# Kernel optimization log

Hardware: AMD Instinct MI355X
Metric: run time of the kernel (lower is better)

Reference implementation:

```python
import jax, jax.numpy as jnp
import numpy as np
from jax import lax

B = 64


def _conv_bn_relu(x, w, cb, s, t):
    # 3x3 conv pad=1 (SAME), eval-mode BN folded to per-channel scale s / shift t, ReLU
    y = lax.conv_general_dilated(x, w, (1, 1), 'SAME',
                                 dimension_numbers=('NCHW', 'OIHW', 'NCHW'))
    y = y + cb[None, :, None, None]
    y = y * s[None, :, None, None] + t[None, :, None, None]
    return jax.nn.relu(y)


def _maxpool(x, k):
    return lax.reduce_window(x, -jnp.inf, lax.max, (1, 1, k, k), (1, 1, k, k), 'VALID')


def _tensor_dlt(H4PT, CornerA):
    # Batched version of the per-sample 8x8 DLT solve (faithful to the original row layout)
    U = CornerA[:, 0::2]            # [B,4]
    V = CornerA[:, 1::2]
    Ud = U + H4PT[:, 0::2]
    Vd = V + H4PT[:, 1::2]
    z = jnp.zeros_like(U)
    o = jnp.ones_like(U)
    r0 = jnp.stack([z, z, z, -U, V, -o, Vd * U, Vd * V], axis=-1)   # [B,4,8]
    r1 = jnp.stack([U, V, o, z, z, z, -Ud * U, -Ud * V], axis=-1)   # [B,4,8]
    A = jnp.stack([r0, r1], axis=2).reshape(U.shape[0], 8, 8)        # interleave rows per point
    bvec = jnp.stack([-Vd, Ud], axis=2).reshape(U.shape[0], 8)
    h = jnp.linalg.solve(A, bvec[..., None])[..., 0]                 # [B,8]
    H = jnp.concatenate([h, jnp.ones((U.shape[0], 1), h.dtype)], axis=1)
    return H.reshape(-1, 3, 3)


def _bilinear_sample(img, xs, ys):
    # img [Hs,Ws]; xs, ys [Ho,Wo]; zeros padding outside (grid_sample semantics)
    Hs, Ws = img.shape
    x0 = jnp.floor(xs)
    y0 = jnp.floor(ys)
    wx = xs - x0
    wy = ys - y0
    x0i = x0.astype(jnp.int32)
    y0i = y0.astype(jnp.int32)

    def gat(yi, xi):
        valid = (xi >= 0) & (xi < Ws) & (yi >= 0) & (yi < Hs)
        v = img[jnp.clip(yi, 0, Hs - 1), jnp.clip(xi, 0, Ws - 1)]
        return jnp.where(valid, v, jnp.zeros((), img.dtype))

    v00 = gat(y0i, x0i)
    v01 = gat(y0i, x0i + 1)
    v10 = gat(y0i + 1, x0i)
    v11 = gat(y0i + 1, x0i + 1)
    return (v00 * (1 - wx) * (1 - wy) + v01 * wx * (1 - wy)
            + v10 * (1 - wx) * wy + v11 * wx * wy)


def _warp_perspective(imgs, Hm, out_hw=(128, 128)):
    # dst(x,y) = src(H^{-1} [x,y,1]); align_corners=True pixel coordinates
    Ho, Wo = out_hw
    dt = imgs.dtype
    ys, xs = jnp.meshgrid(jnp.arange(Ho, dtype=dt), jnp.arange(Wo, dtype=dt), indexing='ij')
    grid = jnp.stack([xs, ys, jnp.ones_like(xs)], axis=-1)           # [Ho,Wo,3]
    Hinv = jnp.linalg.inv(Hm)                                        # [B,3,3]
    pts = jnp.einsum('bij,hwj->bhwi', Hinv, grid)                    # [B,Ho,Wo,3]
    xs_s = pts[..., 0] / pts[..., 2]
    ys_s = pts[..., 1] / pts[..., 2]
    out = jax.vmap(_bilinear_sample)(imgs, xs_s, ys_s)               # [B,Ho,Wo]
    return out[:, None]                                              # [B,1,Ho,Wo]


def setup_inputs() -> dict:
    key = jax.random.key(0)
    ks = jax.random.split(key, 64)
    d = {}
    d['TCropABatch'] = jax.random.uniform(ks[0], (B, 128, 128), jnp.float32)
    d['TI1Batch'] = jax.random.uniform(ks[1], (B, 2, 128, 128), jnp.float32)
    d['TImgABatch'] = jax.random.uniform(ks[2], (B, 240, 320), jnp.float32)
    # corners of a 128x128 quad inside the 240x320 image: (x,y) per corner, 8 values
    x0 = jax.random.uniform(ks[3], (B,), jnp.float32, 0.0, 192.0)
    y0 = jax.random.uniform(ks[4], (B,), jnp.float32, 0.0, 112.0)
    d['TCornerBatch'] = jnp.stack(
        [x0, y0, x0 + 127.0, y0, x0, y0 + 127.0, x0 + 127.0, y0 + 127.0], axis=1)
    chans = [(2, 64), (64, 64), (64, 64), (64, 64), (64, 128), (128, 128), (128, 128), (128, 128)]
    ki = 5
    for i, (ci, co) in enumerate(chans, start=1):
        fan = ci * 9
        d[f'w{i}'] = jax.random.normal(ks[ki], (co, ci, 3, 3), jnp.float32) * np.float32((2.0 / fan) ** 0.5)
        d[f'cb{i}'] = jnp.zeros((co,), jnp.float32)
        d[f's{i}'] = jnp.ones((co,), jnp.float32) + 0.01 * jax.random.normal(ks[ki + 1], (co,), jnp.float32)
        d[f't{i}'] = 0.01 * jax.random.normal(ks[ki + 2], (co,), jnp.float32)
        ki += 3
    d['fcw'] = jax.random.normal(ks[ki], (1024, 512), jnp.float32) * 0.02
    d['fcb'] = jnp.zeros((1024,), jnp.float32)
    d['f1w'] = jax.random.normal(ks[ki + 1], (8, 1024), jnp.float32) * 0.01
    d['f1b'] = jnp.zeros((8,), jnp.float32)
    return d


def reference(TCropABatch, TI1Batch, TImgABatch, TCornerBatch,
              w1, cb1, s1, t1, w2, cb2, s2, t2, w3, cb3, s3, t3, w4, cb4, s4, t4,
              w5, cb5, s5, t5, w6, cb6, s6, t6, w7, cb7, s7, t7, w8, cb8, s8, t8,
              fcw, fcb, f1w, f1b):
    ws = [w1, w2, w3, w4, w5, w6, w7, w8]
    cbs = [cb1, cb2, cb3, cb4, cb5, cb6, cb7, cb8]
    ss = [s1, s2, s3, s4, s5, s6, s7, s8]
    ts = [t1, t2, t3, t4, t5, t6, t7, t8]
    pools = [None, 2, None, 2, None, 2, None, 6]
    out = TI1Batch
    for i in range(8):
        out = _conv_bn_relu(out, ws[i], cbs[i], ss[i], ts[i])
        if pools[i] is not None:
            out = _maxpool(out, pools[i])
    out = out.reshape(out.shape[0], -1)                 # [B,512]
    out = jax.nn.relu(out @ fcw.T + fcb)                # dropout is eval-mode identity
    H4PT = out @ f1w.T + f1b                            # [B,8]
    Hm = _tensor_dlt(H4PT, TCornerBatch)                # [B,3,3]
    b_Pred = _warp_perspective(TImgABatch, Hm)          # [B,1,128,128]
    return b_Pred
```

## Files before the change

### kernel.cpp

```cpp
#include <hip/hip_runtime.h>
#include <math.h>

typedef __attribute__((ext_vector_type(4))) float f32x4;
typedef __attribute__((ext_vector_type(8))) short sh8;

__device__ __forceinline__ float bf2f(unsigned short u){
    union { unsigned int i; float f; } v; v.i = ((unsigned)u) << 16; return v.f;
}
__device__ __forceinline__ unsigned short f2bf(float f){
    union { float f; unsigned int i; } v; v.f = f;
    unsigned int x = v.i;
    x += 0x7fff + ((x >> 16) & 1);
    return (unsigned short)(x >> 16);
}

struct WTArgs {
    const float* src[7];
    unsigned short* hi[7];
    int cin[7];
    int start[8];
};

__global__ void wtrans_all(WTArgs a)
{
    int e = blockIdx.x * 256 + threadIdx.x;
    if (e >= a.start[7]) return;
    int l = 0;
    while (e >= a.start[l + 1]) l++;
    int eL = e - a.start[l];
    int CIN = a.cin[l];
    int tap = eL % 9, rest = eL / 9;
    int ci = rest % CIN, co = rest / CIN;
    int COUT = (a.start[l + 1] - a.start[l]) / (9 * CIN);
    a.hi[l][(tap * COUT + co) * CIN + ci] = f2bf(a.src[l][eL]);
}

__global__ __launch_bounds__(256) void conv1_kernel(
    const float* __restrict__ in, const float* __restrict__ w,
    const float* __restrict__ cb, const float* __restrict__ sc,
    const float* __restrict__ tb, unsigned short* __restrict__ out)
{
    __shared__ float s_w[18 * 64];
    __shared__ float s_in[2][18 * 20];

    const int tid = threadIdx.x;
    const int b = blockIdx.y;
    const int tile = blockIdx.x;
    const int ty = tile >> 3, tx = tile & 7;
    const int y0 = ty * 16, x0 = tx * 16;

    for (int idx = tid; idx < 1152; idx += 256) {
        int co = idx & 63, kk2 = idx >> 6;
        s_w[kk2 * 64 + co] = w[co * 18 + kk2];
    }
    for (int idx = tid; idx < 2 * 324; idx += 256) {
        int ci = idx / 324, rem = idx % 324;
        int r = rem / 18, c = rem % 18;
        int gy = y0 + r - 1, gx = x0 + c - 1;
        float v = 0.f;
        if (gy >= 0 && gy < 128 && gx >= 0 && gx < 128)
            v = in[((size_t)(b * 2 + ci) * 128 + gy) * 128 + gx];
        s_in[ci][r * 20 + c] = v;
    }
    __syncthreads();

    const int cog = tid >> 5;
    const int slot = tid & 31;
    const int sy = slot >> 2, sx = slot & 3;

    float p[2][4][6];
#pragma unroll
    for (int ci = 0; ci < 2; ci++)
#pragma unroll
        for (int r = 0; r < 4; r++)
#pragma unroll
            for (int c = 0; c < 6; c++)
                p[ci][r][c] = s_in[ci][(2 * sy + r) * 20 + 4 * sx + c];

    float acc[2][4][8];
#pragma unroll
    for (int r = 0; r < 2; r++)
#pragma unroll
        for (int c = 0; c < 4; c++)
#pragma unroll
            for (int o = 0; o < 8; o++) acc[r][c][o] = 0.f;

#pragma unroll
    for (int kk2 = 0; kk2 < 18; kk2++) {
        const int ci = kk2 / 9, k = kk2 % 9;
        const int ky = k / 3, kx = k % 3;
        float wv[8];
#pragma unroll
        for (int q = 0; q < 2; q++) {
            f32x4 w4 = *(const f32x4*)(&s_w[kk2 * 64 + cog * 8 + q * 4]);
#pragma unroll
            for (int z = 0; z < 4; z++) wv[q * 4 + z] = w4[z];
        }
#pragma unroll
        for (int r = 0; r < 2; r++)
#pragma unroll
            for (int c = 0; c < 4; c++) {
                float pv = p[ci][r + ky][c + kx];
#pragma unroll
                for (int o = 0; o < 8; o++) acc[r][c][o] += pv * wv[o];
            }
    }

    float bb[8], ss[8], tt[8];
#pragma unroll
    for (int o = 0; o < 8; o++) { bb[o] = cb[cog*8+o]; ss[o] = sc[cog*8+o]; tt[o] = tb[cog*8+o]; }
#pragma unroll
    for (int r = 0; r < 2; r++)
#pragma unroll
        for (int c = 0; c < 4; c++) {
            unsigned short ov[8];
#pragma unroll
            for (int o = 0; o < 8; o++)
                ov[o] = f2bf(fmaxf((acc[r][c][o] + bb[o]) * ss[o] + tt[o], 0.f));
            int py = y0 + 2 * sy + r, px = x0 + 4 * sx + c;
            *(sh8*)(out + ((size_t)(b * 128 + py) * 128 + px) * 64 + cog * 8) = *(sh8*)ov;
        }
}

template<int CIN, int COUT, int HI, int WI, int POOL, int TW, int NPG, int KSPLIT>
__global__ __launch_bounds__(NPG * 128, 4) void conv_mfma(
    const unsigned short* __restrict__ in,
    const unsigned short* __restrict__ wgt,
    const float* __restrict__ cb, const float* __restrict__ sc,
    const float* __restrict__ tb, void* __restrict__ outv)
{
    constexpr int THREADS = NPG * 128;
    constexpr int TH = (TW == 32) ? 2 * NPG : 4 * NPG;
    constexpr int HALW = TW + 2, HALH = TH + 2;
    constexpr int NPIX = HALW * HALH;
    constexpr int CHUNKS = CIN / 64;
    constexpr int TILESX = WI / TW;
    constexpr int HO = HI / POOL, WO = WI / POOL;
    constexpr int ST = 68;
    constexpr int NCOG = COUT / 64;
    constexpr int GPT = 512 / THREADS;
    constexpr int LOG_NPG = (NPG == 4) ? 2 : 1;

    __shared__ __align__(16) unsigned short lds_A[NPIX * ST];
    __shared__ __align__(16) unsigned short lds_W[2][4096];

    const int tid = threadIdx.x;
    const int lane = tid & 63;
    const int i = lane & 15, j = lane >> 4;
    const int wv = tid >> 6;
    const int pg = wv & (NPG - 1);
    const int cg = wv >> LOG_NPG;
    const int tile = blockIdx.x;
    const int ty = tile / TILESX, tx = tile % TILESX;
    const int y0 = ty * TH, x0 = tx * TW;
    const int cogrp = (NCOG == 1) ? 0 : (blockIdx.y & (NCOG - 1));
    const int kc = (KSPLIT == 2) ? (blockIdx.y >> (NCOG == 2 ? 1 : 0)) : 0;
    const int coBase = cogrp * 64;
    const int b = blockIdx.z;

    f32x4 acc[4][2];
#pragma unroll
    for (int pf = 0; pf < 4; pf++)
#pragma unroll
        for (int cf = 0; cf < 2; cf++) acc[pf][cf] = (f32x4){0.f, 0.f, 0.f, 0.f};

    sh8 rw[GPT];

    constexpr int NCH = (KSPLIT == 2) ? 1 : CHUNKS;
    for (int cc = 0; cc < NCH; cc++) {
        const int c = (KSPLIT == 2) ? kc : cc;
        if (cc) __syncthreads();

        for (int u = tid; u < NPIX * 8; u += THREADS) {
            int hp = u >> 3, c16 = u & 7;
            int hy = hp / HALW, hx = hp % HALW;
            int gy = y0 + hy - 1, gx = x0 + hx - 1;
            sh8 v = (sh8){0,0,0,0,0,0,0,0};
            if (gy >= 0 && gy < HI && gx >= 0 && gx < WI)
                v = *(const sh8*)(in + ((size_t)(b * HI + gy) * WI + gx) * CIN + c * 64 + c16 * 8);
            *(sh8*)(&lds_A[hp * ST + c16 * 8]) = v;
        }

        auto LOADW = [&](int tap) {
#pragma unroll
            for (int q = 0; q < GPT; q++) {
                int g = tid + q * THREADS;
                int slot = g & 7;
                int co = g >> 3;
                int gl = slot ^ (co & 7);
                rw[q] = *(const sh8*)(wgt + ((size_t)(tap * COUT + coBase + co)) * CIN
                                      + c * 64 + gl * 8);
            }
        };
        auto WRITEW = [&](int bi) {
#pragma unroll
            for (int q = 0; q < GPT; q++)
                *(sh8*)(&lds_W[bi][(tid + q * THREADS) * 8]) = rw[q];
        };

        LOADW(0); WRITEW(0);
        __syncthreads();

#pragma unroll
        for (int tap = 0; tap < 9; tap++) {
            if (tap < 8) LOADW(tap + 1);
            const int ky = tap / 3, kx = tap % 3;
            const int bi = tap & 1;
#pragma unroll
            for (int kk = 0; kk < 2; kk++) {
                sh8 aF[4], bF[2];
#pragma unroll
                for (int pf = 0; pf < 4; pf++) {
                    const int nf = pg * 4 + pf;
                    int hy2, hx2;
                    if (TW == 32) { hy2 = (nf >> 1) + ky; hx2 = (nf & 1) * 16 + i + kx; }
                    else          { hy2 = nf + ky;        hx2 = i + kx; }
                    aF[pf] = *(const sh8*)(&lds_A[(hy2 * HALW + hx2) * ST + kk * 32 + j * 8]);
                }
#pragma unroll
                for (int cf = 0; cf < 2; cf++) {
                    const int co_l = cg * 32 + cf * 16 + i;
                    const int phys = ((kk << 2) | j) ^ (co_l & 7);
                    bF[cf] = *(const sh8*)(&lds_W[bi][(co_l * 8 + phys) * 8]);
                }
                __builtin_amdgcn_s_setprio(1);
#pragma unroll
                for (int pf = 0; pf < 4; pf++)
#pragma unroll
                    for (int cf = 0; cf < 2; cf++)
                        acc[pf][cf] = __builtin_amdgcn_mfma_f32_16x16x32_bf16(
                            aF[pf], bF[cf], acc[pf][cf], 0, 0, 0);
                __builtin_amdgcn_s_setprio(0);
            }
            if (tap < 8) { WRITEW((tap + 1) & 1); __syncthreads(); }
        }
    }

    if constexpr (KSPLIT == 2) {
        float* po = (float*)outv + (size_t)kc * 64 * HO * WO * COUT;
#pragma unroll
        for (int cf = 0; cf < 2; cf++) {
            const int co = coBase + cg * 32 + cf * 16 + i;
#pragma unroll
            for (int pf = 0; pf < 4; pf++) {
                const int nf = pg * 4 + pf;
                int py, pxb;
                if (TW == 32) { py = nf >> 1; pxb = (nf & 1) * 16; }
                else          { py = nf;      pxb = 0; }
#pragma unroll
                for (int r = 0; r < 4; r++)
                    po[((size_t)(b * HO + y0 + py) * WO + x0 + pxb + j * 4 + r) * COUT + co] =
                        acc[pf][cf][r];
            }
        }
        return;
    }

    unsigned short* out = (unsigned short*)outv;
#pragma unroll
    for (int cf = 0; cf < 2; cf++) {
        const int co = coBase + cg * 32 + cf * 16 + i;
        const float b3 = cb[co], s3 = sc[co], t3 = tb[co];
        if (POOL == 1) {
#pragma unroll
            for (int pf = 0; pf < 4; pf++) {
                const int nf = pg * 4 + pf;
                int py, pxb;
                if (TW == 32) { py = nf >> 1; pxb = (nf & 1) * 16; }
                else          { py = nf;      pxb = 0; }
#pragma unroll
                for (int r = 0; r < 4; r++) {
                    float v = fmaxf((acc[pf][cf][r] + b3) * s3 + t3, 0.f);
                    out[((size_t)(b * HO + y0 + py) * WO + x0 + pxb + j * 4 + r) * COUT + co] = f2bf(v);
                }
            }
        } else if constexpr (POOL == 2 && TW == 32) {
#pragma unroll
            for (int h = 0; h < 2; h++) {
                const int pfA = h, pfB = 2 + h;
#pragma unroll
                for (int r2 = 0; r2 < 2; r2++) {
                    float vA0 = fmaxf((acc[pfA][cf][2*r2]   + b3) * s3 + t3, 0.f);
                    float vA1 = fmaxf((acc[pfA][cf][2*r2+1] + b3) * s3 + t3, 0.f);
                    float vB0 = fmaxf((acc[pfB][cf][2*r2]   + b3) * s3 + t3, 0.f);
                    float vB1 = fmaxf((acc[pfB][cf][2*r2+1] + b3) * s3 + t3, 0.f);
                    float v = fmaxf(fmaxf(vA0, vA1), fmaxf(vB0, vB1));
                    int pox = (x0 >> 1) + h * 8 + j * 2 + r2;
                    int poy = (y0 >> 1) + pg;
                    out[((size_t)(b * HO + poy) * WO + pox) * COUT + co] = f2bf(v);
                }
            }
        }
    }
}

__global__ void combine_k(const float* __restrict__ part, const float* __restrict__ cb,
                          const float* __restrict__ sc, const float* __restrict__ tb,
                          unsigned short* __restrict__ out)
{
    int e = blockIdx.x * 256 + threadIdx.x;
    int co = e & 127;
    float v = part[e] + part[e + 2097152];
    out[e] = f2bf(fmaxf((v + cb[co]) * sc[co] + tb[co], 0.f));
}

__global__ void pool6_kernel(const unsigned short* __restrict__ in, float* __restrict__ out)
{
    int t = blockIdx.x * 256 + threadIdx.x;
    if (t >= 64 * 128 * 4) return;
    int ox = t & 1, oy = (t >> 1) & 1, c = (t >> 2) & 127, b = t >> 9;
    const unsigned short* p = in + ((size_t)(b * 16 + oy * 6) * 16 + ox * 6) * 128 + c;
    float m = -INFINITY;
#pragma unroll
    for (int r = 0; r < 6; r++)
#pragma unroll
        for (int cc = 0; cc < 6; cc++) m = fmaxf(m, bf2f(p[(r * 16 + cc) * 128]));
    out[(size_t)b * 512 + c * 4 + oy * 2 + ox] = m;
}

__global__ void fc1_kernel(const float* __restrict__ flat, const float* __restrict__ fcw,
                           const float* __restrict__ fcb, float* __restrict__ out1)
{
    int b = blockIdx.y;
    int jj = blockIdx.x * 256 + threadIdx.x;
    const f32x4* f = (const f32x4*)(flat + (size_t)b * 512);
    const f32x4* w = (const f32x4*)(fcw + (size_t)jj * 512);
    float s = fcb[jj];
    for (int k = 0; k < 128; k++) {
        f32x4 a = f[k], ww = w[k];
        s += a[0]*ww[0] + a[1]*ww[1] + a[2]*ww[2] + a[3]*ww[3];
    }
    out1[(size_t)b * 1024 + jj] = fmaxf(s, 0.f);
}

__global__ void fc2_kernel(const float* __restrict__ out1, const float* __restrict__ f1w,
                           const float* __restrict__ f1b, float* __restrict__ h4pt)
{
    int b = blockIdx.x;
    int o = threadIdx.x >> 5, s2 = threadIdx.x & 31;
    const float* pa = out1 + (size_t)b * 1024;
    const float* pw = f1w + (size_t)o * 1024;
    float s = 0.f;
    for (int k = s2; k < 1024; k += 32) s += pa[k] * pw[k];
#pragma unroll
    for (int m = 16; m; m >>= 1) s += __shfl_xor(s, m);
    if (s2 == 0) h4pt[b * 8 + o] = s + f1b[o];
}

__global__ void dlt_kernel(const float* __restrict__ h4pt, const float* __restrict__ corner,
                           double* __restrict__ hinv)
{
    int b = threadIdx.x;
    if (b >= 64) return;
    double U[4], V[4], Ud[4], Vd[4];
    for (int jq = 0; jq < 4; jq++) {
        U[jq] = (double)corner[b * 8 + 2 * jq];
        V[jq] = (double)corner[b * 8 + 2 * jq + 1];
        Ud[jq] = U[jq] + (double)h4pt[b * 8 + 2 * jq];
        Vd[jq] = V[jq] + (double)h4pt[b * 8 + 2 * jq + 1];
    }
    double A[8][9];
    for (int jq = 0; jq < 4; jq++) {
        double* r0 = A[2 * jq];
        double* r1 = A[2 * jq + 1];
        r0[0] = 0;     r0[1] = 0;     r0[2] = 0;
        r0[3] = -U[jq]; r0[4] = V[jq]; r0[5] = -1;
        r0[6] = Vd[jq] * U[jq]; r0[7] = Vd[jq] * V[jq]; r0[8] = -Vd[jq];
        r1[0] = U[jq]; r1[1] = V[jq]; r1[2] = 1;
        r1[3] = 0;     r1[4] = 0;     r1[5] = 0;
        r1[6] = -Ud[jq] * U[jq]; r1[7] = -Ud[jq] * V[jq]; r1[8] = Ud[jq];
    }
    for (int col = 0; col < 8; col++) {
        int piv = col; double mx = fabs(A[col][col]);
        for (int r = col + 1; r < 8; r++) {
            double v = fabs(A[r][col]);
            if (v > mx) { mx = v; piv = r; }
        }
        if (piv != col)
            for (int cc = col; cc < 9; cc++) { double tmp = A[col][cc]; A[col][cc] = A[piv][cc]; A[piv][cc] = tmp; }
        double inv = 1.0 / A[col][col];
        for (int r = col + 1; r < 8; r++) {
            double f = A[r][col] * inv;
            for (int cc = col; cc < 9; cc++) A[r][cc] -= f * A[col][cc];
        }
    }
    double h[9];
    for (int r = 7; r >= 0; r--) {
        double s = A[r][8];
        for (int cc = r + 1; cc < 8; cc++) s -= A[r][cc] * h[cc];
        h[r] = s / A[r][r];
    }
    h[8] = 1.0;
    double a = h[0], bb = h[1], cq = h[2], d = h[3], e = h[4], f = h[5], g = h[6], hh = h[7], iq = h[8];
    double C00 = e * iq - f * hh, C01 = cq * hh - bb * iq, C02 = bb * f - cq * e;
    double C10 = f * g - d * iq,  C11 = a * iq - cq * g,   C12 = cq * d - a * f;
    double C20 = d * hh - e * g,  C21 = bb * g - a * hh,   C22 = a * e - bb * d;
    double det = a * C00 + bb * C10 + cq * C20;
    double idet = 1.0 / det;
    double* o = hinv + b * 9;
    o[0] = C00 * idet; o[1] = C01 * idet; o[2] = C02 * idet;
    o[3] = C10 * idet; o[4] = C11 * idet; o[5] = C12 * idet;
    o[6] = C20 * idet; o[7] = C21 * idet; o[8] = C22 * idet;
}

__global__ void warp_kernel(const float* __restrict__ img, const double* __restrict__ hinv,
                            float* __restrict__ out)
{
    int b = blockIdx.y;
    int pix = blockIdx.x * 256 + threadIdx.x;
    int y = pix >> 7, x = pix & 127;
    const double* h = hinv + b * 9;
    double X = (double)x, Y = (double)y;
    double p0 = h[0] * X + h[1] * Y + h[2];
    double p1 = h[3] * X + h[4] * Y + h[5];
    double p2 = h[6] * X + h[7] * Y + h[8];
    double xs = p0 / p2, ys = p1 / p2;
    double x0d = floor(xs), y0d = floor(ys);
    double wx = xs - x0d, wy = ys - y0d;
    int x0 = (int)x0d, y0 = (int)y0d;
    const float* im = img + (size_t)b * 240 * 320;
    auto gat = [&](int yi, int xi) -> double {
        bool valid = (xi >= 0) & (xi < 320) & (yi >= 0) & (yi < 240);
        int yc = yi < 0 ? 0 : (yi > 239 ? 239 : yi);
        int xc = xi < 0 ? 0 : (xi > 319 ? 319 : xi);
        double v = (double)im[yc * 320 + xc];
        return valid ? v : 0.0;
    };
    double v00 = gat(y0, x0),     v01 = gat(y0, x0 + 1);
    double v10 = gat(y0 + 1, x0), v11 = gat(y0 + 1, x0 + 1);
    double r = v00 * (1 - wx) * (1 - wy) + v01 * wx * (1 - wy)
             + v10 * (1 - wx) * wy       + v11 * wx * wy;
    out[((size_t)b << 14) + pix] = (float)r;
}

extern "C" void kernel_launch(void* const* d_in, const int* in_sizes, int n_in,
                              void* d_out, int out_size, void* d_ws, size_t ws_size,
                              hipStream_t stream)
{
    const float* TI1     = (const float*)d_in[1];
    const float* TImgA   = (const float*)d_in[2];
    const float* TCorner = (const float*)d_in[3];
    const float* w[8], *cbp[8], *sp[8], *tp[8];
    for (int l = 0; l < 8; l++) {
        w[l]   = (const float*)d_in[4 + 4 * l];
        cbp[l] = (const float*)d_in[5 + 4 * l];
        sp[l]  = (const float*)d_in[6 + 4 * l];
        tp[l]  = (const float*)d_in[7 + 4 * l];
    }
    const float* fcw = (const float*)d_in[36];
    const float* fcb = (const float*)d_in[37];
    const float* f1w = (const float*)d_in[38];
    const float* f1b = (const float*)d_in[39];

    char* base = (char*)d_ws;
    unsigned short* A    = (unsigned short*)(base);
    unsigned short* Bb   = (unsigned short*)(base + 33554432);
    unsigned short* whiA = (unsigned short*)(base + 67108864);
    float*  feat = (float*) (base + 67108864 + 1253376);
    float*  fc1o = feat + 64 * 512;
    float*  h4pt = fc1o + 64 * 1024;
    double* hinv = (double*)(h4pt + 512);
    float*  outp = (float*)d_out;

    float*          part7   = (float*)A;
    unsigned short* c7out   = (unsigned short*)(base + 33554432 + 8388608);
    float*          part8   = (float*)A;
    unsigned short* c8out   = (unsigned short*)(base + 33554432 + 16777216);

    const int CINS[7]  = {64, 64, 64, 64, 128, 128, 128};
    const int COUTS[7] = {64, 64, 64, 128, 128, 128, 128};
    int wofs[8]; wofs[0] = 0;
    for (int l = 0; l < 7; l++) wofs[l + 1] = wofs[l] + 9 * COUTS[l] * CINS[l];

    WTArgs wa;
    for (int l = 0; l < 7; l++) {
        wa.src[l] = w[l + 1];
        wa.hi[l] = whiA + wofs[l];
        wa.cin[l] = CINS[l];
        wa.start[l] = wofs[l];
    }
    wa.start[7] = wofs[7];
    wtrans_all<<<(wofs[7] + 255) / 256, 256, 0, stream>>>(wa);

    for (int ch = 0; ch < 4; ch++) {
        conv1_kernel<<<dim3(64, 16), 256, 0, stream>>>(
            TI1 + (size_t)ch * 16 * 2 * 128 * 128, w[0], cbp[0], sp[0], tp[0], A);
        conv_mfma<64, 64, 128, 128, 2, 32, 4, 1><<<dim3(64, 1, 16), 512, 0, stream>>>(
            A, whiA + wofs[0], cbp[1], sp[1], tp[1],
            Bb + (size_t)ch * 16 * 64 * 64 * 64);
    }
    conv_mfma<64, 64, 64, 64, 1, 32, 4, 1><<<dim3(16, 1, 64), 512, 0, stream>>>(
        Bb, whiA + wofs[1], cbp[2], sp[2], tp[2], A);
    conv_mfma<64, 64, 64, 64, 2, 32, 4, 1><<<dim3(16, 1, 64), 512, 0, stream>>>(
        A, whiA + wofs[2], cbp[3], sp[3], tp[3], Bb);
    conv_mfma<64, 128, 32, 32, 1, 32, 4, 1><<<dim3(4, 2, 64), 512, 0, stream>>>(
        Bb, whiA + wofs[3], cbp[4], sp[4], tp[4], A);
    conv_mfma<128, 128, 32, 32, 2, 32, 4, 1><<<dim3(4, 2, 64), 512, 0, stream>>>(
        A, whiA + wofs[4], cbp[5], sp[5], tp[5], Bb);
    conv_mfma<128, 128, 16, 16, 1, 16, 2, 2><<<dim3(2, 4, 64), 256, 0, stream>>>(
        Bb, whiA + wofs[5], cbp[6], sp[6], tp[6], part7);
    combine_k<<<8192, 256, 0, stream>>>(part7, cbp[6], sp[6], tp[6], c7out);
    conv_mfma<128, 128, 16, 16, 1, 16, 2, 2><<<dim3(2, 4, 64), 256, 0, stream>>>(
        c7out, whiA + wofs[6], cbp[7], sp[7], tp[7], part8);
    combine_k<<<8192, 256, 0, stream>>>(part8, cbp[7], sp[7], tp[7], c8out);

    pool6_kernel<<<128, 256, 0, stream>>>(c8out, feat);
    fc1_kernel<<<dim3(4, 64), 256, 0, stream>>>(feat, fcw, fcb, fc1o);
    fc2_kernel<<<64, 256, 0, stream>>>(fc1o, f1w, f1b, h4pt);
    dlt_kernel<<<1, 64, 0, stream>>>(h4pt, TCorner, hinv);
    warp_kernel<<<dim3(64, 64), 256, 0, stream>>>(TImgA, hinv, outp);
}
```

Before: 367.5 us.

## Move conv1 to MFMA via im2col and retile conv_mfma to 256 threads

The first 2-channel conv is rewritten as an im2col GEMM with K padded to 32. It builds bf16 patches in LDS from a halo tile and issues MFMA instructions, replacing the scalar FP32 FMA loop; a new kernel pre-packs the conv1 weights. The generic conv_mfma kernel is restructured to 256 threads, with each wave covering all 64 output channels (4x4 accumulators) and the input channel dimension chunked by 32 instead of 64. This halves the LDS tiles but doubles the number of chunk iterations and barriers. The split-K layers now use one spatial tile per block and loop over multiple chunks.

```diff
diff --git a/kernel.cpp b/kernel.cpp
--- a/kernel.cpp
+++ b/kernel.cpp
@@ -35,167 +35,180 @@
     a.hi[l][(tap * COUT + co) * CIN + ci] = f2bf(a.src[l][eL]);
 }
 
-__global__ __launch_bounds__(256) void conv1_kernel(
-    const float* __restrict__ in, const float* __restrict__ w,
+__global__ void wtrans1(const float* __restrict__ w1, unsigned short* __restrict__ wB)
+{
+    int e = blockIdx.x * 256 + threadIdx.x;
+    if (e >= 2048) return;
+    int co = e >> 5, k = e & 31;
+    float v = 0.f;
+    if (k < 18) { int tap = k >> 1, ci = k & 1; v = w1[co * 18 + ci * 9 + tap]; }
+    wB[e] = f2bf(v);
+}
+
+__global__ __launch_bounds__(256, 4) void conv1_mfma(
+    const float* __restrict__ in,
+    const unsigned short* __restrict__ wB,
     const float* __restrict__ cb, const float* __restrict__ sc,
     const float* __restrict__ tb, unsigned short* __restrict__ out)
 {
-    __shared__ float s_w[18 * 64];
-    __shared__ float s_in[2][18 * 20];
+    __shared__ float s_halo[2][10 * 36];
+    __shared__ __align__(16) unsigned short s_A[256 * 40];
+    __shared__ __align__(16) unsigned short s_W[2048];
 
     const int tid = threadIdx.x;
+    const int lane = tid & 63;
+    const int i = lane & 15, j = lane >> 4;
+    const int pg = tid >> 6;
     const int b = blockIdx.y;
     const int tile = blockIdx.x;
-    const int ty = tile >> 3, tx = tile & 7;
-    const int y0 = ty * 16, x0 = tx * 16;
-
-    for (int idx = tid; idx < 1152; idx += 256) {
-        int co = idx & 63, kk2 = idx >> 6;
-        s_w[kk2 * 64 + co] = w[co * 18 + kk2];
-    }
-    for (int idx = tid; idx < 2 * 324; idx += 256) {
-        int ci = idx / 324, rem = idx % 324;
-        int r = rem / 18, c = rem % 18;
-        int gy = y0 + r - 1, gx = x0 + c - 1;
+    const int ty = tile >> 2, tx = tile & 3;
+    const int y0 = ty * 8, x0 = tx * 32;
+
+    for (int idx = tid; idx < 680; idx += 256) {
+        int ci = idx >= 340 ? 1 : 0;
+        int rem = idx - ci * 340;
+        int r = rem / 34, c2 = rem % 34;
+        int gy = y0 + r - 1, gx = x0 + c2 - 1;
         float v = 0.f;
         if (gy >= 0 && gy < 128 && gx >= 0 && gx < 128)
             v = in[((size_t)(b * 2 + ci) * 128 + gy) * 128 + gx];
-        s_in[ci][r * 20 + c] = v;
+        s_halo[ci][r * 36 + c2] = v;
+    }
+    {
+        int row = tid >> 3, phys = tid & 7;
+        int s8l = phys ^ (row & 7);
+        int co = row * 2 + (s8l >> 2), g = s8l & 3;
+        *(sh8*)(&s_W[tid * 8]) = *(const sh8*)(wB + co * 32 + g * 8);
     }
     __syncthreads();
 
-    const int cog = tid >> 5;
-    const int slot = tid & 31;
-    const int sy = slot >> 2, sx = slot & 3;
-
-    float p[2][4][6];
-#pragma unroll
-    for (int ci = 0; ci < 2; ci++)
-#pragma unroll
-        for (int r = 0; r < 4; r++)
-#pragma unroll
-            for (int c = 0; c < 6; c++)
-                p[ci][r][c] = s_in[ci][(2 * sy + r) * 20 + 4 * sx + c];
-
-    float acc[2][4][8];
-#pragma unroll
-    for (int r = 0; r < 2; r++)
-#pragma unroll
-        for (int c = 0; c < 4; c++)
-#pragma unroll
-            for (int o = 0; o < 8; o++) acc[r][c][o] = 0.f;
-
-#pragma unroll
-    for (int kk2 = 0; kk2 < 18; kk2++) {
-        const int ci = kk2 / 9, k = kk2 % 9;
-        const int ky = k / 3, kx = k % 3;
-        float wv[8];
-#pragma unroll
-        for (int q = 0; q < 2; q++) {
-            f32x4 w4 = *(const f32x4*)(&s_w[kk2 * 64 + cog * 8 + q * 4]);
-#pragma unroll
-            for (int z = 0; z < 4; z++) wv[q * 4 + z] = w4[z];
-        }
-#pragma unroll
-        for (int r = 0; r < 2; r++)
-#pragma unroll
-            for (int c = 0; c < 4; c++) {
-                float pv = p[ci][r + ky][c + kx];
-#pragma unroll
-                for (int o = 0; o < 8; o++) acc[r][c][o] += pv * wv[o];
-            }
-    }
-
-    float bb[8], ss[8], tt[8];
-#pragma unroll
-    for (int o = 0; o < 8; o++) { bb[o] = cb[cog*8+o]; ss[o] = sc[cog*8+o]; tt[o] = tb[cog*8+o]; }
-#pragma unroll
-    for (int r = 0; r < 2; r++)
-#pragma unroll
-        for (int c = 0; c < 4; c++) {
-            unsigned short ov[8];
-#pragma unroll
-            for (int o = 0; o < 8; o++)
-                ov[o] = f2bf(fmaxf((acc[r][c][o] + bb[o]) * ss[o] + tt[o], 0.f));
-            int py = y0 + 2 * sy + r, px = x0 + 4 * sx + c;
-            *(sh8*)(out + ((size_t)(b * 128 + py) * 128 + px) * 64 + cog * 8) = *(sh8*)ov;
-        }
-}
-
-template<int CIN, int COUT, int HI, int WI, int POOL, int TW, int NPG, int KSPLIT>
-__global__ __launch_bounds__(NPG * 128, 4) void conv_mfma(
+    {
+        const int px = tid, pr = px >> 5, pc = px & 31;
+        sh8 rr[4];
+#pragma unroll
+        for (int g = 0; g < 4; g++)
+#pragma unroll
+            for (int m = 0; m < 8; m++) {
+                const int k = g * 8 + m;
+                unsigned short val = 0;
+                if (k < 18) {
+                    const int tap = k >> 1, ci = k & 1;
+                    val = f2bf(s_halo[ci][(pr + tap / 3) * 36 + pc + tap % 3]);
+                }
+                rr[g][m] = (short)val;
+            }
+#pragma unroll
+        for (int g = 0; g < 4; g++)
+            *(sh8*)(&s_A[px * 40 + g * 8]) = rr[g];
+    }
+    __syncthreads();
+
+    f32x4 acc[4][4];
+#pragma unroll
+    for (int pf = 0; pf < 4; pf++)
+#pragma unroll
+        for (int cf = 0; cf < 4; cf++) acc[pf][cf] = (f32x4){0.f, 0.f, 0.f, 0.f};
+
+    sh8 aF[4], bF[4];
+#pragma unroll
+    for (int pf = 0; pf < 4; pf++) {
+        const int nf = pg * 4 + pf;
+        const int px = (nf >> 1) * 32 + (nf & 1) * 16 + i;
+        aF[pf] = *(const sh8*)(&s_A[px * 40 + j * 8]);
+    }
+#pragma unroll
+    for (int cf = 0; cf < 4; cf++) {
+        const int co_l = cf * 16 + i;
+        const int roww = co_l >> 1;
+        const int phys = ((co_l & 1) * 4 + j) ^ (roww & 7);
+        bF[cf] = *(const sh8*)(&s_W[(roww * 8 + phys) * 8]);
+    }
+#pragma unroll
+    for (int pf = 0; pf < 4; pf++)
+#pragma unroll
+        for (int cf = 0; cf < 4; cf++)
+            acc[pf][cf] = __builtin_amdgcn_mfma_f32_16x16x32_bf16(aF[pf], bF[cf], acc[pf][cf], 0, 0, 0);
+
+#pragma unroll
+    for (int cf = 0; cf < 4; cf++) {
+        const int co = cf * 16 + i;
+        const float b3 = cb[co], s3 = sc[co], t3 = tb[co];
+#pragma unroll
+        for (int pf = 0; pf < 4; pf++) {
+            const int nf = pg * 4 + pf;
+            const int py = y0 + (nf >> 1);
+            const int pxb = x0 + (nf & 1) * 16;
+#pragma unroll
+            for (int r = 0; r < 4; r++) {
+                float v = fmaxf((acc[pf][cf][r] + b3) * s3 + t3, 0.f);
+                out[((size_t)(b * 128 + py) * 128 + pxb + j * 4 + r) * 64 + co] = f2bf(v);
+            }
+        }
+    }
+}
+
+template<int CIN, int COUT, int HI, int WI, int POOL, int TW, int KSPLIT>
+__global__ __launch_bounds__(256, 4) void conv_mfma(
     const unsigned short* __restrict__ in,
     const unsigned short* __restrict__ wgt,
     const float* __restrict__ cb, const float* __restrict__ sc,
     const float* __restrict__ tb, void* __restrict__ outv)
 {
-    constexpr int THREADS = NPG * 128;
-    constexpr int TH = (TW == 32) ? 2 * NPG : 4 * NPG;
+    constexpr int TH = 256 / TW;
     constexpr int HALW = TW + 2, HALH = TH + 2;
     constexpr int NPIX = HALW * HALH;
-    constexpr int CHUNKS = CIN / 64;
+    constexpr int CHUNKS = CIN / 32;
     constexpr int TILESX = WI / TW;
     constexpr int HO = HI / POOL, WO = WI / POOL;
-    constexpr int ST = 68;
+    constexpr int ST = 36;
     constexpr int NCOG = COUT / 64;
-    constexpr int GPT = 512 / THREADS;
-    constexpr int LOG_NPG = (NPG == 4) ? 2 : 1;
 
     __shared__ __align__(16) unsigned short lds_A[NPIX * ST];
-    __shared__ __align__(16) unsigned short lds_W[2][4096];
+    __shared__ __align__(16) unsigned short lds_W[2][2048];
 
     const int tid = threadIdx.x;
     const int lane = tid & 63;
     const int i = lane & 15, j = lane >> 4;
-    const int wv = tid >> 6;
-    const int pg = wv & (NPG - 1);
-    const int cg = wv >> LOG_NPG;
+    const int pg = tid >> 6;
     const int tile = blockIdx.x;
     const int ty = tile / TILESX, tx = tile % TILESX;
     const int y0 = ty * TH, x0 = tx * TW;
-    const int cogrp = (NCOG == 1) ? 0 : (blockIdx.y & (NCOG - 1));
-    const int kc = (KSPLIT == 2) ? (blockIdx.y >> (NCOG == 2 ? 1 : 0)) : 0;
+    const int cogrp = (NCOG == 2) ? (blockIdx.y & 1) : 0;
+    const int kc = (KSPLIT == 2) ? ((int)blockIdx.y >> (NCOG - 1)) : 0;
     const int coBase = cogrp * 64;
     const int b = blockIdx.z;
 
-    f32x4 acc[4][2];
+    f32x4 acc[4][4];
 #pragma unroll
     for (int pf = 0; pf < 4; pf++)
 #pragma unroll
-        for (int cf = 0; cf < 2; cf++) acc[pf][cf] = (f32x4){0.f, 0.f, 0.f, 0.f};
-
-    sh8 rw[GPT];
-
-    constexpr int NCH = (KSPLIT == 2) ? 1 : CHUNKS;
+        for (int cf = 0; cf < 4; cf++) acc[pf][cf] = (f32x4){0.f, 0.f, 0.f, 0.f};
+
+    sh8 rw;
+    constexpr int NCH = (KSPLIT == 2) ? CHUNKS / 2 : CHUNKS;
+
     for (int cc = 0; cc < NCH; cc++) {
-        const int c = (KSPLIT == 2) ? kc : cc;
+        const int c = (KSPLIT == 2) ? kc * NCH + cc : cc;
         if (cc) __syncthreads();
 
-        for (int u = tid; u < NPIX * 8; u += THREADS) {
-            int hp = u >> 3, c16 = u & 7;
+        for (int u = tid; u < NPIX * 4; u += 256) {
+            int hp = u >> 2, c16 = u & 3;
             int hy = hp / HALW, hx = hp % HALW;
             int gy = y0 + hy - 1, gx = x0 + hx - 1;
             sh8 v = (sh8){0,0,0,0,0,0,0,0};
             if (gy >= 0 && gy < HI && gx >= 0 && gx < WI)
-                v = *(const sh8*)(in + ((size_t)(b * HI + gy) * WI + gx) * CIN + c * 64 + c16 * 8);
+                v = *(const sh8*)(in + ((size_t)(b * HI + gy) * WI + gx) * CIN + c * 32 + c16 * 8);
             *(sh8*)(&lds_A[hp * ST + c16 * 8]) = v;
         }
 
         auto LOADW = [&](int tap) {
-#pragma unroll
-            for (int q = 0; q < GPT; q++) {
-                int g = tid + q * THREADS;
-                int slot = g & 7;
-                int co = g >> 3;
-                int gl = slot ^ (co & 7);
-                rw[q] = *(const sh8*)(wgt + ((size_t)(tap * COUT + coBase + co)) * CIN
-                                      + c * 64 + gl * 8);
-            }
+            int row = tid >> 3, phys = tid & 7;
+            int s8l = phys ^ (row & 7);
+            int co = row * 2 + (s8l >> 2), g = s8l & 3;
+            rw = *(const sh8*)(wgt + ((size_t)(tap * COUT + coBase + co)) * CIN + c * 32 + g * 8);
         };
         auto WRITEW = [&](int bi) {
-#pragma unroll
-            for (int q = 0; q < GPT; q++)
-                *(sh8*)(&lds_W[bi][(tid + q * THREADS) * 8]) = rw[q];
+            *(sh8*)(&lds_W[bi][tid * 8]) = rw;
         };
 
         LOADW(0); WRITEW(0);
@@ -206,32 +219,30 @@
             if (tap < 8) LOADW(tap + 1);
             const int ky = tap / 3, kx = tap % 3;
             const int bi = tap & 1;
-#pragma unroll
-            for (int kk = 0; kk < 2; kk++) {
-                sh8 aF[4], bF[2];
-#pragma unroll
-                for (int pf = 0; pf < 4; pf++) {
-                    const int nf = pg * 4 + pf;
-                    int hy2, hx2;
-                    if (TW == 32) { hy2 = (nf >> 1) + ky; hx2 = (nf & 1) * 16 + i + kx; }
-                    else          { hy2 = nf + ky;        hx2 = i + kx; }
-                    aF[pf] = *(const sh8*)(&lds_A[(hy2 * HALW + hx2) * ST + kk * 32 + j * 8]);
-                }
-#pragma unroll
-                for (int cf = 0; cf < 2; cf++) {
-                    const int co_l = cg * 32 + cf * 16 + i;
-                    const int phys = ((kk << 2) | j) ^ (co_l & 7);
-                    bF[cf] = *(const sh8*)(&lds_W[bi][(co_l * 8 + phys) * 8]);
-                }
-                __builtin_amdgcn_s_setprio(1);
-#pragma unroll
-                for (int pf = 0; pf < 4; pf++)
-#pragma unroll
-                    for (int cf = 0; cf < 2; cf++)
-                        acc[pf][cf] = __builtin_amdgcn_mfma_f32_16x16x32_bf16(
-                            aF[pf], bF[cf], acc[pf][cf], 0, 0, 0);
-                __builtin_amdgcn_s_setprio(0);
-            }
+            sh8 aF[4], bF[4];
+#pragma unroll
+            for (int pf = 0; pf < 4; pf++) {
+                const int nf = pg * 4 + pf;
+                int hy2, hx2;
+                if (TW == 32) { hy2 = (nf >> 1) + ky; hx2 = (nf & 1) * 16 + i + kx; }
+                else          { hy2 = nf + ky;        hx2 = i + kx; }
+                aF[pf] = *(const sh8*)(&lds_A[(hy2 * HALW + hx2) * ST + j * 8]);
+            }
+#pragma unroll
+            for (int cf = 0; cf < 4; cf++) {
+                const int co_l = cf * 16 + i;
+                const int roww = co_l >> 1;
+                const int phys = ((co_l & 1) * 4 + j) ^ (roww & 7);
+                bF[cf] = *(const sh8*)(&lds_W[bi][(roww * 8 + phys) * 8]);
+            }
+            __builtin_amdgcn_s_setprio(1);
+#pragma unroll
+            for (int pf = 0; pf < 4; pf++)
+#pragma unroll
+                for (int cf = 0; cf < 4; cf++)
+                    acc[pf][cf] = __builtin_amdgcn_mfma_f32_16x16x32_bf16(
+                        aF[pf], bF[cf], acc[pf][cf], 0, 0, 0);
+            __builtin_amdgcn_s_setprio(0);
             if (tap < 8) { WRITEW((tap + 1) & 1); __syncthreads(); }
         }
     }
@@ -239,8 +250,8 @@
     if constexpr (KSPLIT == 2) {
         float* po = (float*)outv + (size_t)kc * 64 * HO * WO * COUT;
 #pragma unroll
-        for (int cf = 0; cf < 2; cf++) {
-            const int co = coBase + cg * 32 + cf * 16 + i;
+        for (int cf = 0; cf < 4; cf++) {
+            const int co = coBase + cf * 16 + i;
 #pragma unroll
             for (int pf = 0; pf < 4; pf++) {
                 const int nf = pg * 4 + pf;
@@ -258,8 +269,8 @@
 
     unsigned short* out = (unsigned short*)outv;
 #pragma unroll
-    for (int cf = 0; cf < 2; cf++) {
-        const int co = coBase + cg * 32 + cf * 16 + i;
+    for (int cf = 0; cf < 4; cf++) {
+        const int co = coBase + cf * 16 + i;
         const float b3 = cb[co], s3 = sc[co], t3 = tb[co];
         if (POOL == 1) {
 #pragma unroll
@@ -456,7 +467,8 @@
     unsigned short* A    = (unsigned short*)(base);
     unsigned short* Bb   = (unsigned short*)(base + 33554432);
     unsigned short* whiA = (unsigned short*)(base + 67108864);
-    float*  feat = (float*) (base + 67108864 + 1253376);
+    unsigned short* wB1  = whiA + 626688;
+    float*  feat = (float*) (base + 67108864 + 1253376 + 4096);
     float*  fc1o = feat + 64 * 512;
     float*  h4pt = fc1o + 64 * 1024;
     double* hinv = (double*)(h4pt + 512);
@@ -481,26 +493,27 @@
     }
     wa.start[7] = wofs[7];
     wtrans_all<<<(wofs[7] + 255) / 256, 256, 0, stream>>>(wa);
+    wtrans1<<<8, 256, 0, stream>>>(w[0], wB1);
 
     for (int ch = 0; ch < 4; ch++) {
-        conv1_kernel<<<dim3(64, 16), 256, 0, stream>>>(
-            TI1 + (size_t)ch * 16 * 2 * 128 * 128, w[0], cbp[0], sp[0], tp[0], A);
-        conv_mfma<64, 64, 128, 128, 2, 32, 4, 1><<<dim3(64, 1, 16), 512, 0, stream>>>(
+        conv1_mfma<<<dim3(64, 16), 256, 0, stream>>>(
+            TI1 + (size_t)ch * 16 * 2 * 128 * 128, wB1, cbp[0], sp[0], tp[0], A);
+        conv_mfma<64, 64, 128, 128, 2, 32, 1><<<dim3(64, 1, 16), 256, 0, stream>>>(
             A, whiA + wofs[0], cbp[1], sp[1], tp[1],
             Bb + (size_t)ch * 16 * 64 * 64 * 64);
     }
-    conv_mfma<64, 64, 64, 64, 1, 32, 4, 1><<<dim3(16, 1, 64), 512, 0, stream>>>(
+    conv_mfma<64, 64, 64, 64, 1, 32, 1><<<dim3(16, 1, 64), 256, 0, stream>>>(
         Bb, whiA + wofs[1], cbp[2], sp[2], tp[2], A);
-    conv_mfma<64, 64, 64, 64, 2, 32, 4, 1><<<dim3(16, 1, 64), 512, 0, stream>>>(
+    conv_mfma<64, 64, 64, 64, 2, 32, 1><<<dim3(16, 1, 64), 256, 0, stream>>>(
         A, whiA + wofs[2], cbp[3], sp[3], tp[3], Bb);
-    conv_mfma<64, 128, 32, 32, 1, 32, 4, 1><<<dim3(4, 2, 64), 512, 0, stream>>>(
+    conv_mfma<64, 128, 32, 32, 1, 32, 1><<<dim3(4, 2, 64), 256, 0, stream>>>(
         Bb, whiA + wofs[3], cbp[4], sp[4], tp[4], A);
-    conv_mfma<128, 128, 32, 32, 2, 32, 4, 1><<<dim3(4, 2, 64), 512, 0, stream>>>(
+    conv_mfma<128, 128, 32, 32, 2, 32, 1><<<dim3(4, 2, 64), 256, 0, stream>>>(
         A, whiA + wofs[4], cbp[5], sp[5], tp[5], Bb);
-    conv_mfma<128, 128, 16, 16, 1, 16, 2, 2><<<dim3(2, 4, 64), 256, 0, stream>>>(
+    conv_mfma<128, 128, 16, 16, 1, 16, 2><<<dim3(1, 4, 64), 256, 0, stream>>>(
         Bb, whiA + wofs[5], cbp[6], sp[6], tp[6], part7);
     combine_k<<<8192, 256, 0, stream>>>(part7, cbp[6], sp[6], tp[6], c7out);
-    conv_mfma<128, 128, 16, 16, 1, 16, 2, 2><<<dim3(2, 4, 64), 256, 0, stream>>>(
+    conv_mfma<128, 128, 16, 16, 1, 16, 2><<<dim3(1, 4, 64), 256, 0, stream>>>(
         c7out, whiA + wofs[6], cbp[7], sp[7], tp[7], part8);
     combine_k<<<8192, 256, 0, stream>>>(part8, cbp[7], sp[7], tp[7], c8out);
 
```

Result: slower. 445.4 us (+21.2%).

## Parallelize DLT solve across lanes and merge batch-chunked first convs

Applied to the files above, without the earlier changes.

The DLT kernel now assigns one matrix row per lane (8 lanes per sample, 512 threads), doing partial pivoting and elimination with wave shuffles instead of a serial 8x9 double-precision solve per thread. Separately, the four-chunk loop of conv1 and conv2 launches is replaced by single full-batch launches, with the workspace buffers enlarged to hold the full activations. This cuts launch count and the long serial latency of the single-thread-per-sample solver, at the cost of a larger workspace footprint and more memory traffic between conv1 and conv2.

```diff
diff --git a/kernel.cpp b/kernel.cpp
--- a/kernel.cpp
+++ b/kernel.cpp
@@ -347,60 +347,77 @@
     if (s2 == 0) h4pt[b * 8 + o] = s + f1b[o];
 }
 
-__global__ void dlt_kernel(const float* __restrict__ h4pt, const float* __restrict__ corner,
-                           double* __restrict__ hinv)
-{
-    int b = threadIdx.x;
-    if (b >= 64) return;
-    double U[4], V[4], Ud[4], Vd[4];
-    for (int jq = 0; jq < 4; jq++) {
-        U[jq] = (double)corner[b * 8 + 2 * jq];
-        V[jq] = (double)corner[b * 8 + 2 * jq + 1];
-        Ud[jq] = U[jq] + (double)h4pt[b * 8 + 2 * jq];
-        Vd[jq] = V[jq] + (double)h4pt[b * 8 + 2 * jq + 1];
-    }
-    double A[8][9];
-    for (int jq = 0; jq < 4; jq++) {
-        double* r0 = A[2 * jq];
-        double* r1 = A[2 * jq + 1];
-        r0[0] = 0;     r0[1] = 0;     r0[2] = 0;
-        r0[3] = -U[jq]; r0[4] = V[jq]; r0[5] = -1;
-        r0[6] = Vd[jq] * U[jq]; r0[7] = Vd[jq] * V[jq]; r0[8] = -Vd[jq];
-        r1[0] = U[jq]; r1[1] = V[jq]; r1[2] = 1;
-        r1[3] = 0;     r1[4] = 0;     r1[5] = 0;
-        r1[6] = -Ud[jq] * U[jq]; r1[7] = -Ud[jq] * V[jq]; r1[8] = Ud[jq];
-    }
+__global__ __launch_bounds__(512) void dlt_kernel(
+    const float* __restrict__ h4pt, const float* __restrict__ corner,
+    double* __restrict__ hinv)
+{
+    const int t = threadIdx.x;
+    const int lane = t & 63;
+    const int r = lane & 7;
+    const int base = lane & ~7;
+    const int b = (t >> 6) * 8 + (lane >> 3);
+
+    const int jq = r >> 1;
+    const double U  = (double)corner[b * 8 + 2 * jq];
+    const double V  = (double)corner[b * 8 + 2 * jq + 1];
+    const double Ud = U + (double)h4pt[b * 8 + 2 * jq];
+    const double Vd = V + (double)h4pt[b * 8 + 2 * jq + 1];
+
+    double Ar[9];
+    if ((r & 1) == 0) {
+        Ar[0] = 0;  Ar[1] = 0;  Ar[2] = 0;
+        Ar[3] = -U; Ar[4] = V;  Ar[5] = -1;
+        Ar[6] = Vd * U; Ar[7] = Vd * V; Ar[8] = -Vd;
+    } else {
+        Ar[0] = U;  Ar[1] = V;  Ar[2] = 1;
+        Ar[3] = 0;  Ar[4] = 0;  Ar[5] = 0;
+        Ar[6] = -Ud * U; Ar[7] = -Ud * V; Ar[8] = Ud;
+    }
+
+#pragma unroll
     for (int col = 0; col < 8; col++) {
-        int piv = col; double mx = fabs(A[col][col]);
-        for (int r = col + 1; r < 8; r++) {
-            double v = fabs(A[r][col]);
-            if (v > mx) { mx = v; piv = r; }
-        }
-        if (piv != col)
-            for (int cc = col; cc < 9; cc++) { double tmp = A[col][cc]; A[col][cc] = A[piv][cc]; A[piv][cc] = tmp; }
-        double inv = 1.0 / A[col][col];
-        for (int r = col + 1; r < 8; r++) {
-            double f = A[r][col] * inv;
-            for (int cc = col; cc < 9; cc++) A[r][cc] -= f * A[col][cc];
-        }
-    }
+        double val = (r >= col) ? fabs(Ar[col]) : -1.0;
+        int idx = r;
+#pragma unroll
+        for (int m = 1; m < 8; m <<= 1) {
+            double ov = __shfl_xor(val, m, 64);
+            int oi = __shfl_xor(idx, m, 64);
+            if (ov > val || (ov == val && oi < idx)) { val = ov; idx = oi; }
+        }
+        const int src = (r == col) ? idx : (r == idx) ? col : r;
+#pragma unroll
+        for (int k = 0; k < 9; k++) Ar[k] = __shfl(Ar[k], base + src, 64);
+        double pr[9];
+#pragma unroll
+        for (int k = 0; k < 9; k++) pr[k] = __shfl(Ar[k], base + col, 64);
+        if (r > col) {
+            const double f = Ar[col] / pr[col];
+#pragma unroll
+            for (int k = 0; k < 9; k++) Ar[k] -= f * pr[k];
+        }
+    }
+
     double h[9];
-    for (int r = 7; r >= 0; r--) {
-        double s = A[r][8];
-        for (int cc = r + 1; cc < 8; cc++) s -= A[r][cc] * h[cc];
-        h[r] = s / A[r][r];
-    }
     h[8] = 1.0;
-    double a = h[0], bb = h[1], cq = h[2], d = h[3], e = h[4], f = h[5], g = h[6], hh = h[7], iq = h[8];
-    double C00 = e * iq - f * hh, C01 = cq * hh - bb * iq, C02 = bb * f - cq * e;
-    double C10 = f * g - d * iq,  C11 = a * iq - cq * g,   C12 = cq * d - a * f;
-    double C20 = d * hh - e * g,  C21 = bb * g - a * hh,   C22 = a * e - bb * d;
-    double det = a * C00 + bb * C10 + cq * C20;
-    double idet = 1.0 / det;
+#pragma unroll
+    for (int col = 7; col >= 0; col--) {
+        const double xc = __shfl(Ar[8] / Ar[col], base + col, 64);
+        h[col] = xc;
+        if (r < col) Ar[8] -= Ar[col] * xc;
+    }
+
+    const double a = h[0], bb = h[1], cq = h[2], d = h[3], e = h[4],
+                 f = h[5], g = h[6], hh = h[7], iq = h[8];
+    const double C0 = e * iq - f * hh, C1 = cq * hh - bb * iq, C2 = bb * f - cq * e;
+    const double C3 = f * g - d * iq,  C4 = a * iq - cq * g,   C5 = cq * d - a * f;
+    const double C6 = d * hh - e * g,  C7 = bb * g - a * hh,   C8 = a * e - bb * d;
+    const double det = a * C0 + bb * C3 + cq * C6;
+    const double idet = 1.0 / det;
+    double my = (r == 0) ? C0 : (r == 1) ? C1 : (r == 2) ? C2 : (r == 3) ? C3
+              : (r == 4) ? C4 : (r == 5) ? C5 : (r == 6) ? C6 : C7;
     double* o = hinv + b * 9;
-    o[0] = C00 * idet; o[1] = C01 * idet; o[2] = C02 * idet;
-    o[3] = C10 * idet; o[4] = C11 * idet; o[5] = C12 * idet;
-    o[6] = C20 * idet; o[7] = C21 * idet; o[8] = C22 * idet;
+    o[r] = my * idet;
+    if (r == 0) o[8] = C8 * idet;
 }
 
 __global__ void warp_kernel(const float* __restrict__ img, const double* __restrict__ hinv,
@@ -428,9 +445,9 @@
     };
     double v00 = gat(y0, x0),     v01 = gat(y0, x0 + 1);
     double v10 = gat(y0 + 1, x0), v11 = gat(y0 + 1, x0 + 1);
-    double r = v00 * (1 - wx) * (1 - wy) + v01 * wx * (1 - wy)
-             + v10 * (1 - wx) * wy       + v11 * wx * wy;
-    out[((size_t)b << 14) + pix] = (float)r;
+    double rr = v00 * (1 - wx) * (1 - wy) + v01 * wx * (1 - wy)
+              + v10 * (1 - wx) * wy       + v11 * wx * wy;
+    out[((size_t)b << 14) + pix] = (float)rr;
 }
 
 extern "C" void kernel_launch(void* const* d_in, const int* in_sizes, int n_in,
@@ -453,19 +470,19 @@
     const float* f1b = (const float*)d_in[39];
 
     char* base = (char*)d_ws;
-    unsigned short* A    = (unsigned short*)(base);
-    unsigned short* Bb   = (unsigned short*)(base + 33554432);
-    unsigned short* whiA = (unsigned short*)(base + 67108864);
-    float*  feat = (float*) (base + 67108864 + 1253376);
+    unsigned short* A1   = (unsigned short*)(base);
+    unsigned short* B2   = (unsigned short*)(base + 134217728);
+    unsigned short* whiA = (unsigned short*)(base + 167772160);
+    float*  feat = (float*) (base + 167772160 + 1253376);
     float*  fc1o = feat + 64 * 512;
     float*  h4pt = fc1o + 64 * 1024;
     double* hinv = (double*)(h4pt + 512);
     float*  outp = (float*)d_out;
 
-    float*          part7   = (float*)A;
-    unsigned short* c7out   = (unsigned short*)(base + 33554432 + 8388608);
-    float*          part8   = (float*)A;
-    unsigned short* c8out   = (unsigned short*)(base + 33554432 + 16777216);
+    float*          part7 = (float*)A1;
+    unsigned short* c7out = (unsigned short*)(base + 134217728 + 8388608);
+    float*          part8 = (float*)A1;
+    unsigned short* c8out = (unsigned short*)(base + 134217728 + 16777216);
 
     const int CINS[7]  = {64, 64, 64, 64, 128, 128, 128};
     const int COUTS[7] = {64, 64, 64, 128, 128, 128, 128};
@@ -482,23 +499,20 @@
     wa.start[7] = wofs[7];
     wtrans_all<<<(wofs[7] + 255) / 256, 256, 0, stream>>>(wa);
 
-    for (int ch = 0; ch < 4; ch++) {
-        conv1_kernel<<<dim3(64, 16), 256, 0, stream>>>(
-            TI1 + (size_t)ch * 16 * 2 * 128 * 128, w[0], cbp[0], sp[0], tp[0], A);
-        conv_mfma<64, 64, 128, 128, 2, 32, 4, 1><<<dim3(64, 1, 16), 512, 0, stream>>>(
-            A, whiA + wofs[0], cbp[1], sp[1], tp[1],
-            Bb + (size_t)ch * 16 * 64 * 64 * 64);
-    }
+    conv1_kernel<<<dim3(64, 64), 256, 0, stream>>>(
+        TI1, w[0], cbp[0], sp[0], tp[0], A1);
+    conv_mfma<64, 64, 128, 128, 2, 32, 4, 1><<<dim3(64, 1, 64), 512, 0, stream>>>(
+        A1, whiA + wofs[0], cbp[1], sp[1], tp[1], B2);
     conv_mfma<64, 64, 64, 64, 1, 32, 4, 1><<<dim3(16, 1, 64), 512, 0, stream>>>(
-        Bb, whiA + wofs[1], cbp[2], sp[2], tp[2], A);
+        B2, whiA + wofs[1], cbp[2], sp[2], tp[2], A1);
     conv_mfma<64, 64, 64, 64, 2, 32, 4, 1><<<dim3(16, 1, 64), 512, 0, stream>>>(
-        A, whiA + wofs[2], cbp[3], sp[3], tp[3], Bb);
+        A1, whiA + wofs[2], cbp[3], sp[3], tp[3], B2);
     conv_mfma<64, 128, 32, 32, 1, 32, 4, 1><<<dim3(4, 2, 64), 512, 0, stream>>>(
-        Bb, whiA + wofs[3], cbp[4], sp[4], tp[4], A);
+        B2, whiA + wofs[3], cbp[4], sp[4], tp[4], A1);
     conv_mfma<128, 128, 32, 32, 2, 32, 4, 1><<<dim3(4, 2, 64), 512, 0, stream>>>(
-        A, whiA + wofs[4], cbp[5], sp[5], tp[5], Bb);
+        A1, whiA + wofs[4], cbp[5], sp[5], tp[5], B2);
     conv_mfma<128, 128, 16, 16, 1, 16, 2, 2><<<dim3(2, 4, 64), 256, 0, stream>>>(
-        Bb, whiA + wofs[5], cbp[6], sp[6], tp[6], part7);
+        B2, whiA + wofs[5], cbp[6], sp[6], tp[6], part7);
     combine_k<<<8192, 256, 0, stream>>>(part7, cbp[6], sp[6], tp[6], c7out);
     conv_mfma<128, 128, 16, 16, 1, 16, 2, 2><<<dim3(2, 4, 64), 256, 0, stream>>>(
         c7out, whiA + wofs[6], cbp[7], sp[7], tp[7], part8);
@@ -507,6 +521,6 @@
     pool6_kernel<<<128, 256, 0, stream>>>(c8out, feat);
     fc1_kernel<<<dim3(4, 64), 256, 0, stream>>>(feat, fcw, fcb, fc1o);
     fc2_kernel<<<64, 256, 0, stream>>>(fc1o, f1w, f1b, h4pt);
-    dlt_kernel<<<1, 64, 0, stream>>>(h4pt, TCorner, hinv);
+    dlt_kernel<<<1, 512, 0, stream>>>(h4pt, TCorner, hinv);
     warp_kernel<<<dim3(64, 64), 256, 0, stream>>>(TImgA, hinv, outp);
 }
```

Measured after the change: 319.5 us. -13.1%, faster.
